# Kernel optimization log

Hardware: AMD Instinct MI355X
Metric: run time of the kernel (lower is better)

## Reference

```python
import jax, jax.numpy as jnp
import numpy as np

B, C, L, H, K, NCONV = 16, 128, 1024, 8, 7, 4
DK = C // H
EPS = 1e-5
NEG = -1e30


def setup_inputs() -> dict:
    key = jax.random.key(0)
    ks = jax.random.split(key, 20)
    s = 0.05
    rn = lambda k, shape: jax.random.normal(k, shape, jnp.float32) * s
    return {
        "x": jax.random.normal(ks[0], (B, C, L), jnp.float32),
        "mask": jax.random.bernoulli(ks[1], 0.1, (B, L)),
        "dw_w": rn(ks[2], (NCONV, C, K)),
        "pw_w": rn(ks[3], (NCONV, C, C)),
        "pw_b": rn(ks[4], (NCONV, C)),
        "ng": jnp.ones((NCONV + 2, C), jnp.float32),
        "nb": jnp.zeros((NCONV + 2, C), jnp.float32),
        "wq": rn(ks[5], (C, C)), "bq": rn(ks[6], (C,)),
        "wk": rn(ks[7], (C, C)), "bk": rn(ks[8], (C,)),
        "wv": rn(ks[9], (C, C)), "bv": rn(ks[10], (C,)),
        "wo": rn(ks[11], (C, C)), "bo": rn(ks[12], (C,)),
        "w1": rn(ks[13], (C, C)), "b1": rn(ks[14], (C,)),
        "w2": rn(ks[15], (C, C)), "b2": rn(ks[16], (C,)),
    }


def _pos_encoding(c, length):
    i = jnp.arange(c, dtype=jnp.float32)
    even = (jnp.arange(c) % 2) == 0
    freq = jnp.where(even, jnp.power(10000.0, -i / c), -jnp.power(10000.0, (1.0 - i) / c))
    phase = jnp.where(even, 0.0, jnp.pi / 2)
    pos = jnp.arange(length, dtype=jnp.float32)
    return jnp.sin(pos[None, :] * freq[:, None] + phase[:, None])  # [C, L]


def _ln(x, g, b):
    # layer norm over channel dim of [B, C, L]
    mu = jnp.mean(x, axis=1, keepdims=True)
    var = jnp.mean(jnp.square(x - mu), axis=1, keepdims=True)
    xn = (x - mu) * jax.lax.rsqrt(var + EPS)
    return xn * g[None, :, None] + b[None, :, None]


def _dsconv(x, dw, pw, pb):
    # depthwise conv1d (groups=C, pad k//2, no bias) + pointwise conv1d (bias)
    y = jax.lax.conv_general_dilated(
        x, dw[:, None, :], window_strides=(1,), padding=[(K // 2, K // 2)],
        feature_group_count=C, dimension_numbers=("NCH", "OIH", "NCH"))
    return jnp.einsum("oc,bcl->bol", pw, y) + pb[None, :, None]


def _attention(x, mask, wq, bq, wk, bk, wv, bv, wo, bo):
    # x: [B, C, L] -> [B, L, C]
    xt = jnp.swapaxes(x, 1, 2)
    q = (xt @ wq.T + bq).reshape(B, L, H, DK)
    k = (xt @ wk.T + bk).reshape(B, L, H, DK)
    v = (xt @ wv.T + bv).reshape(B, L, H, DK)
    scale = 1.0 / np.sqrt(DK)
    scores = jnp.einsum("blhd,bmhd->bhlm", q, k) * scale  # [B, H, L, L]
    scores = jnp.where(mask[:, None, None, :], NEG, scores)
    attn = jax.nn.softmax(scores, axis=-1)
    out = jnp.einsum("bhlm,bmhd->blhd", attn, v).reshape(B, L, C)
    out = out @ wo.T + bo
    return jnp.swapaxes(out, 1, 2)  # [B, C, L]


def reference(x, mask, dw_w, pw_w, pw_b, ng, nb, wq, bq, wk, bk, wv, bv, wo, bo, w1, b1, w2, b2):
    # eval mode: all dropout / stochastic depth are identity
    out = x + _pos_encoding(C, L)[None]
    for i in range(NCONV):
        res = out
        out = _ln(out, ng[i], nb[i])
        out = _dsconv(out, dw_w[i], pw_w[i], pw_b[i])
        out = jax.nn.relu(out)
        out = out + res
    res = out
    out = _ln(out, ng[NCONV], nb[NCONV])
    out = _attention(out, mask, wq, bq, wk, bk, wv, bv, wo, bo)
    out = out + res
    res = out
    out = _ln(out, ng[NCONV + 1], nb[NCONV + 1])
    ot = jnp.swapaxes(out, 1, 2)
    ot = jax.nn.relu(ot @ w1.T + b1)
    ot = ot @ w2.T + b2
    out = jnp.swapaxes(ot, 1, 2) + res
    return out
```

## Files before the change

kernel.cpp:

```cpp
#include <hip/hip_runtime.h>
#include <math.h>


#define ACT_N   2097152
#define OFF_ACT0 0
#define OFF_ACT1 (ACT_N)
#define OFF_QB   (2*ACT_N)
#define OFF_KB   (3*ACT_N)
#define OFF_VT   (4*ACT_N)
#define OFF_ABF  (5*ACT_N)
#define OFF_MF   (6*ACT_N)
#define OFF_WB   (6*ACT_N + 16384)
#define OFF_DW8  (6*ACT_N + 16384 + 81920)

typedef __attribute__((ext_vector_type(8)))  short bf16x8;
typedef __attribute__((ext_vector_type(16))) float f32x16;
typedef __attribute__((ext_vector_type(4)))  float f32x4;

static __device__ __forceinline__ unsigned int f2bf(float f) {
    unsigned int u = __float_as_uint(f);
    return (u + 0x7fffu + ((u >> 16) & 1u)) >> 16;
}
static __device__ __forceinline__ unsigned int pk2(float a, float b) {
    return f2bf(a) | (f2bf(b) << 16);
}

#define GOFF(row, g) (((row) << 8) + ((((g) ^ ((row) & 15))) << 4))

#define QSCALE 0.3606737602222409f

__global__ __launch_bounds__(256) void k_prep(
    const float* __restrict__ pw, const float* __restrict__ wq,
    const float* __restrict__ wk, const float* __restrict__ wv_,
    const float* __restrict__ wo, const float* __restrict__ w1,
    const float* __restrict__ w2, const unsigned char* __restrict__ mask,
    const float* __restrict__ dwsrc,
    unsigned short* __restrict__ wb, float* __restrict__ maskf,
    float* __restrict__ dw8)
{
    int blk = blockIdx.x, t = threadIdx.x;
    if (blk < 10) {
        const float* src;
        if (blk < 4)       src = pw + blk * 16384;
        else if (blk == 4) src = wq;
        else if (blk == 5) src = wk;
        else if (blk == 6) src = wv_;
        else if (blk == 7) src = wo;
        else if (blk == 8) src = w1;
        else               src = w2;
        unsigned short* dst = wb + blk * 16384;
        for (int i = t * 8; i < 16384; i += 2048) {
            float4 a = *(const float4*)(src + i);
            float4 c = *(const float4*)(src + i + 4);
            uint4 v;
            v.x = pk2(a.x, a.y); v.y = pk2(a.z, a.w);
            v.z = pk2(c.x, c.y); v.w = pk2(c.z, c.w);
            *(uint4*)(dst + i) = v;
        }
    } else if (blk == 10) {
        for (int i = t; i < 16384; i += 256)
            maskf[i] = mask[i] ? -3.0e38f : 0.0f;
    } else {
        for (int i = t; i < 4096; i += 256) {
            int n = i >> 3, tap = i & 7;
            dw8[i] = (tap < 7) ? dwsrc[n * 7 + tap] : 0.0f;
        }
    }
}

__global__ __launch_bounds__(256) void k_pe(const float* __restrict__ x,
                                            float* __restrict__ out)
{
    int i4 = blockIdx.x * 256 + threadIdx.x;
    int base = i4 * 4;
    int l = base & 1023;
    int c = (base >> 10) & 127;
    float e = (float)(c & ~1);
    float fb = exp2f(e * (-13.287712379549449f / 128.0f));
    float freq = (c & 1) ? -fb : fb;
    float ph   = (c & 1) ? 1.5707963267948966f : 0.0f;
    float4 xv = ((const float4*)x)[i4];
    float4 o;
    o.x = xv.x + sinf((float)l * freq + ph);
    o.y = xv.y + sinf((float)(l + 1) * freq + ph);
    o.z = xv.z + sinf((float)(l + 2) * freq + ph);
    o.w = xv.w + sinf((float)(l + 3) * freq + ph);
    ((float4*)out)[i4] = o;
}

__global__ __launch_bounds__(512) void k_conv(
    const float* __restrict__ in, float* __restrict__ out,
    const unsigned short* __restrict__ wb,
    const float* __restrict__ dw8,
    const float* __restrict__ pb,
    const float* __restrict__ g, const float* __restrict__ nbv)
{
    __shared__ unsigned short Wl[16384];
    __shared__ unsigned short Xl[8192];
    __shared__ float part[560];
    __shared__ float muL[70], rsL[70];

    const int b  = blockIdx.x >> 4;
    const int l0 = (blockIdx.x & 15) << 6;
    const int t  = threadIdx.x;
    const int lane = t & 63;
    const int w = __builtin_amdgcn_readfirstlane(t >> 6);
    const float* xb = in + b * 131072;

    {
        const uint4* src = (const uint4*)wb;
        #pragma unroll
        for (int i = 0; i < 4; ++i) {
            int gi = t + i * 512;
            uint4 v = src[gi];
            int row = gi >> 4, c16 = gi & 15;
            *(uint4*)((char*)Wl + GOFF(row, c16)) = v;
        }
    }
    if (t < 280) {
        int col = t >> 2, sl = t & 3;
        int gl = l0 - 3 + col;
        float s = 0.f, ss = 0.f;
        if ((unsigned)gl < 1024u) {
            for (int c = sl * 32; c < sl * 32 + 32; ++c) {
                float v = xb[c * 1024 + gl];
                s += v; ss = fmaf(v, v, ss);
            }
        }
        part[col * 8 + sl * 2]     = s;
        part[col * 8 + sl * 2 + 1] = ss;
    }
    __syncthreads();
    if (t < 70) {
        int gl = l0 - 3 + t;
        if ((unsigned)gl < 1024u) {
            float s  = part[t*8] + part[t*8+2] + part[t*8+4] + part[t*8+6];
            float ss = part[t*8+1] + part[t*8+3] + part[t*8+5] + part[t*8+7];
            float mu = s * 0.0078125f;
            float var = ss * 0.0078125f - mu * mu;
            muL[t] = mu; rsL[t] = rsqrtf(var + 1e-5f);
        } else { muL[t] = 0.f; rsL[t] = 0.f; }
    }
    __syncthreads();

    {
        const int l = lane;
        const int gl = l0 + l;
        float m[7], rf[7], vm[7];
        int pofs[7];
        #pragma unroll
        for (int j = 0; j < 7; ++j) {
            int p = gl - 3 + j;
            m[j]  = muL[l + j];
            rf[j] = rsL[l + j];
            vm[j] = ((unsigned)p < 1024u) ? 1.f : 0.f;
            pofs[j] = min(max(p, 0), 1023);
        }
        #pragma unroll
        for (int s = 0; s < 2; ++s) {
            int c0 = w * 16 + s * 8;
            unsigned int pk[4];
            #pragma unroll
            for (int cp = 0; cp < 4; ++cp) {
                float y2[2];
                #pragma unroll
                for (int ci = 0; ci < 2; ++ci) {
                    int c = c0 + cp * 2 + ci;
                    const float* xr = xb + c * 1024;
                    const float* dr = dw8 + c * 8;
                    float S1 = 0.f, S2 = 0.f;
                    #pragma unroll
                    for (int j = 0; j < 7; ++j) {
                        float xv = xr[pofs[j]];
                        float u = (xv - m[j]) * rf[j];
                        float dwv = dr[j];
                        S1 = fmaf(dwv, u,     S1);
                        S2 = fmaf(dwv, vm[j], S2);
                    }
                    y2[ci] = g[c] * S1 + nbv[c] * S2;
                }
                pk[cp] = pk2(y2[0], y2[1]);
            }
            *(uint4*)((char*)Xl + GOFF(l, (c0 >> 3))) = *(uint4*)pk;
        }
    }
    __syncthreads();

    const int l31 = lane & 31, hi = lane >> 5;
    const int ow = w >> 1, lh = w & 1;
    bf16x8 af[8];
    #pragma unroll
    for (int kc = 0; kc < 8; ++kc)
        af[kc] = *(const bf16x8*)((char*)Wl + GOFF(ow * 32 + l31, kc * 2 + hi));
    f32x16 acc;
    #pragma unroll
    for (int i = 0; i < 16; ++i) acc[i] = 0.f;
    #pragma unroll
    for (int kc = 0; kc < 8; ++kc) {
        bf16x8 bx = *(const bf16x8*)((char*)Xl + GOFF(lh * 32 + l31, kc * 2 + hi));
        acc = __builtin_amdgcn_mfma_f32_32x32x16_bf16(af[kc], bx, acc, 0, 0, 0);
    }
    float* ob = out + b * 131072;
    const int lg = l0 + lh * 32 + l31;
    #pragma unroll
    for (int r = 0; r < 16; ++r) {
        int o = ow * 32 + (r & 3) + 8 * (r >> 2) + 4 * hi;
        ob[o * 1024 + lg] = fmaxf(acc[r] + pb[o], 0.f) + xb[o * 1024 + lg];
    }
}

__global__ __launch_bounds__(512) void k_qkv(
    const float* __restrict__ in, const unsigned short* __restrict__ wb,
    const float* __restrict__ bq, const float* __restrict__ bk,
    const float* __restrict__ bv,
    const float* __restrict__ g, const float* __restrict__ nbv,
    unsigned short* __restrict__ qb, unsigned short* __restrict__ kb,
    unsigned short* __restrict__ vt)
{
    __shared__ unsigned short Wl[16384];
    __shared__ unsigned short Xl[8192];
    __shared__ unsigned short vs[8][1280];
    __shared__ float part[1024];
    __shared__ float muL[64], rsL[64];

    const int b  = blockIdx.x >> 4;
    const int l0 = (blockIdx.x & 15) << 6;
    const int t  = threadIdx.x;
    const int lane = t & 63;
    const int w = __builtin_amdgcn_readfirstlane(t >> 6);
    const float* xb = in + b * 131072;

    {
        const uint4* src = (const uint4*)wb;
        #pragma unroll
        for (int i = 0; i < 4; ++i) {
            int gi = t + i * 512;
            uint4 v = src[gi];
            int row = gi >> 4, c16 = gi & 15;
            *(uint4*)((char*)Wl + GOFF(row, c16)) = v;
        }
    }
    {
        int col = t >> 3, sl = t & 7;
        float s = 0.f, ss = 0.f;
        for (int c = sl * 16; c < sl * 16 + 16; ++c) {
            float v = xb[c * 1024 + l0 + col];
            s += v; ss = fmaf(v, v, ss);
        }
        part[col * 16 + sl * 2]     = s;
        part[col * 16 + sl * 2 + 1] = ss;
    }
    __syncthreads();
    if (t < 64) {
        float s = 0.f, ss = 0.f;
        #pragma unroll
        for (int j = 0; j < 8; ++j) { s += part[t*16 + j*2]; ss += part[t*16 + j*2 + 1]; }
        float mu = s * 0.0078125f;
        float var = ss * 0.0078125f - mu * mu;
        muL[t] = mu; rsL[t] = rsqrtf(var + 1e-5f);
    }
    __syncthreads();
    {
        const int l = lane;
        float mu = muL[l], rs = rsL[l];
        #pragma unroll
        for (int s = 0; s < 2; ++s) {
            int c0 = w * 16 + s * 8;
            unsigned int pk[4];
            #pragma unroll
            for (int cp = 0; cp < 4; ++cp) {
                int c = c0 + cp * 2;
                float v0 = (xb[c * 1024 + l0 + l]       - mu) * rs * g[c]     + nbv[c];
                float v1 = (xb[(c + 1) * 1024 + l0 + l] - mu) * rs * g[c + 1] + nbv[c + 1];
                pk[cp] = pk2(v0, v1);
            }
            *(uint4*)((char*)Xl + GOFF(l, (c0 >> 3))) = *(uint4*)pk;
        }
    }
    __syncthreads();

    const int l31 = lane & 31, hi = lane >> 5;
    const int ow = w >> 1, lh = w & 1;
    const int lg = l0 + lh * 32 + l31;

    for (int p = 0; p < 3; ++p) {
        uint4 pw4[4];
        if (p < 2) {
            const uint4* src = (const uint4*)(wb + (p + 1) * 16384);
            #pragma unroll
            for (int i = 0; i < 4; ++i) pw4[i] = src[t + i * 512];
        }
        bf16x8 af[8];
        #pragma unroll
        for (int kc = 0; kc < 8; ++kc)
            af[kc] = *(const bf16x8*)((char*)Wl + GOFF(ow * 32 + l31, kc * 2 + hi));
        f32x16 acc;
        #pragma unroll
        for (int i = 0; i < 16; ++i) acc[i] = 0.f;
        #pragma unroll
        for (int kc = 0; kc < 8; ++kc) {
            bf16x8 bx = *(const bf16x8*)((char*)Xl + GOFF(lh * 32 + l31, kc * 2 + hi));
            acc = __builtin_amdgcn_mfma_f32_32x32x16_bf16(af[kc], bx, acc, 0, 0, 0);
        }

        if (p < 2) {
            const float* bias = (p == 0) ? bq : bk;
            unsigned short* dst = (p == 0) ? qb : kb;
            const float scl = (p == 0) ? QSCALE : 1.0f;
            unsigned int pk0[4], pk1[4];
            #pragma unroll
            for (int j2 = 0; j2 < 4; ++j2) {
                int r = j2 * 2;
                int o0 = ow * 32 + (r & 3) + 8 * (r >> 2) + 4 * hi;
                pk0[j2] = pk2((acc[r] + bias[o0]) * scl,
                              (acc[r + 1] + bias[o0 + 1]) * scl);
                int r8 = r + 8;
                int o1 = ow * 32 + (r8 & 3) + 8 * (r8 >> 2) + 4 * hi;
                pk1[j2] = pk2((acc[r8] + bias[o1]) * scl,
                              (acc[r8 + 1] + bias[o1 + 1]) * scl);
            }
            int bh0 = b * 8 + 2 * ow;
            *(uint4*)(dst + ((size_t)bh0 * 1024 + lg) * 16 + hi * 8) = *(uint4*)pk0;
            *(uint4*)(dst + ((size_t)(bh0 + 1) * 1024 + lg) * 16 + hi * 8) = *(uint4*)pk1;
        } else {
            unsigned short* vsw = vs[w];
            #pragma unroll
            for (int r = 0; r < 16; ++r) {
                int orow = (r & 3) + 8 * (r >> 2) + 4 * hi;
                int o = ow * 32 + orow;
                vsw[orow * 40 + l31] = (unsigned short)f2bf(acc[r] + bv[o]);
            }
            int d32 = l31;
            uint4 v0 = *(uint4*)(vsw + d32 * 40 + hi * 16);
            uint4 v1 = *(uint4*)(vsw + d32 * 40 + hi * 16 + 8);
            int head = 2 * ow + (d32 >> 4), dd = d32 & 15;
            unsigned short* vp = vt + ((size_t)(b * 8 + head) * 16 + dd) * 1024
                                    + l0 + lh * 32 + hi * 16;
            *(uint4*)vp = v0; *(uint4*)(vp + 8) = v1;
        }
        __syncthreads();
        if (p < 2) {
            #pragma unroll
            for (int i = 0; i < 4; ++i) {
                int gi = t + i * 512;
                int row = gi >> 4, c16 = gi & 15;
                *(uint4*)((char*)Wl + GOFF(row, c16)) = pw4[i];
            }
            __syncthreads();
        }
    }
}

__global__ __launch_bounds__(256) void k_attn(
    const unsigned short* __restrict__ qb, const unsigned short* __restrict__ kb,
    const unsigned short* __restrict__ vt, const float* __restrict__ madd,
    unsigned short* __restrict__ abf)
{
    __shared__ unsigned short Kl[2][4096];
    __shared__ unsigned short Vl[2][4224];
    __shared__ float Ml[1024];
    __shared__ unsigned int Pl[4][640];

    const int bh = blockIdx.x >> 3;
    const int b  = bh >> 3;
    const int h  = bh & 7;
    const int qbase = (blockIdx.x & 7) << 7;
    const int t = threadIdx.x;
    const int lane = t & 63;
    const int w = t >> 6;
    const int l31 = lane & 31, hi = lane >> 5;
    const int l15 = lane & 15, h2 = lane >> 4;
    const int qw = qbase + w * 32;

    const uint4* ksrc = (const uint4*)(kb + (size_t)bh * 16384);
    const unsigned short* vsrc = vt + (size_t)bh * 16384;

    const int d0v = t >> 5,          ko0 = t & 31;
    const int d1v = (t + 256) >> 5,  ko1 = (t + 256) & 31;
    const int kp0 = t & 1,        kk0 = t >> 1;
    const int kp1 = t & 1,        kk1 = (t + 256) >> 1;

    ((float4*)Ml)[t] = ((const float4*)(madd + b * 1024))[t];

    bf16x8 qf;
    {
        uint4 qv = *(const uint4*)(qb + ((size_t)bh * 1024 + qw + l31) * 16 + hi * 8);
        union { uint4 u; bf16x8 v; } cvt; cvt.u = qv; qf = cvt.v;
    }
    bf16x8 ones;
    #pragma unroll
    for (int i = 0; i < 8; ++i) ones[i] = (short)0x3F80;

    {
        uint4 kr0 = ksrc[t], kr1 = ksrc[t + 256];
        uint4 vr0 = *(const uint4*)(vsrc + d0v * 1024 + ko0 * 8);
        uint4 vr1 = *(const uint4*)(vsrc + d1v * 1024 + ko1 * 8);
        *(uint4*)(&Kl[0][kp0 * 2048 + kk0 * 8]) = kr0;
        *(uint4*)(&Kl[0][kp1 * 2048 + kk1 * 8]) = kr1;
        *(uint4*)(&Vl[0][d0v * 264 + ko0 * 8]) = vr0;
        *(uint4*)(&Vl[0][d1v * 264 + ko1 * 8]) = vr1;
    }
    __syncthreads();

    f32x16 Z;
    #pragma unroll
    for (int i = 0; i < 16; ++i) Z[i] = 0.f;
    f32x4 O0, O1, Os0, Os1;
    #pragma unroll
    for (int i = 0; i < 4; ++i) { O0[i] = 0.f; O1[i] = 0.f; Os0[i] = 0.f; Os1[i] = 0.f; }

    unsigned int* myP = &Pl[w][0];
    int cur = 0;

    for (int ch = 0; ch < 4; ++ch) {
        uint4 kr0, kr1, vr0, vr1;
        if (ch < 3) {
            int cb = (ch + 1) * 512;
            int vb = (ch + 1) * 256;
            kr0 = ksrc[cb + t];
            kr1 = ksrc[cb + t + 256];
            vr0 = *(const uint4*)(vsrc + d0v * 1024 + vb + ko0 * 8);
            vr1 = *(const uint4*)(vsrc + d1v * 1024 + vb + ko1 * 8);
        }
        const unsigned short* Kb = Kl[cur];
        const unsigned short* Vb = Vl[cur];
        const int kgbase = ch * 256;

        #pragma unroll 2
        for (int kc = 0; kc < 8; ++kc) {
            bf16x8 kf = *(const bf16x8*)(Kb + hi * 2048 + (kc * 32 + l31) * 8);
            f32x16 S = __builtin_amdgcn_mfma_f32_32x32x16_bf16(kf, qf, Z, 0, 0, 0);

            #pragma unroll
            for (int rg = 0; rg < 4; ++rg) {
                float4 mm = *(const float4*)(Ml + kgbase + kc * 32 + rg * 8 + hi * 4);
                float p0 = exp2f(S[rg * 4 + 0] + mm.x);
                float p1 = exp2f(S[rg * 4 + 1] + mm.y);
                float p2 = exp2f(S[rg * 4 + 2] + mm.z);
                float p3 = exp2f(S[rg * 4 + 3] + mm.w);
                uint2 pwd;
                pwd.x = __builtin_amdgcn_perm(__float_as_uint(p1),
                                              __float_as_uint(p0), 0x07060302u);
                pwd.y = __builtin_amdgcn_perm(__float_as_uint(p3),
                                              __float_as_uint(p2), 0x07060302u);
                *(uint2*)((char*)myP + l31 * 80 + rg * 16 + hi * 8) = pwd;
            }

            bf16x8 vf  = *(const bf16x8*)(Vb + l15 * 264 + kc * 32 + h2 * 8);
            bf16x8 pa0 = *(const bf16x8*)((const char*)myP + l15 * 80 + h2 * 16);
            bf16x8 pa1 = *(const bf16x8*)((const char*)myP + (16 + l15) * 80 + h2 * 16);
            O0  = __builtin_amdgcn_mfma_f32_16x16x32_bf16(pa0, vf,   O0,  0, 0, 0);
            O1  = __builtin_amdgcn_mfma_f32_16x16x32_bf16(pa1, vf,   O1,  0, 0, 0);
            Os0 = __builtin_amdgcn_mfma_f32_16x16x32_bf16(pa0, ones, Os0, 0, 0, 0);
            Os1 = __builtin_amdgcn_mfma_f32_16x16x32_bf16(pa1, ones, Os1, 0, 0, 0);
        }

        if (ch < 3) {
            __syncthreads();
            int nxt = cur ^ 1;
            *(uint4*)(&Kl[nxt][kp0 * 2048 + kk0 * 8]) = kr0;
            *(uint4*)(&Kl[nxt][kp1 * 2048 + kk1 * 8]) = kr1;
            *(uint4*)(&Vl[nxt][d0v * 264 + ko0 * 8]) = vr0;
            *(uint4*)(&Vl[nxt][d1v * 264 + ko1 * 8]) = vr1;
            __syncthreads();
            cur = nxt;
        }
    }

    unsigned short* myP16 = (unsigned short*)myP;
    #pragma unroll
    for (int r = 0; r < 4; ++r) {
        float i0 = __builtin_amdgcn_rcpf(Os0[r] + 1e-37f);
        float i1 = __builtin_amdgcn_rcpf(Os1[r] + 1e-37f);
        myP16[(h2 * 4 + r) * 20 + l15]        = (unsigned short)f2bf(O0[r] * i0);
        myP16[(16 + h2 * 4 + r) * 20 + l15]   = (unsigned short)f2bf(O1[r] * i1);
    }
    uint4 ov = *(const uint4*)(myP16 + l31 * 20 + hi * 8);
    *(uint4*)(abf + ((size_t)(b * 1024 + qw + l31)) * 128 + h * 16 + hi * 8) = ov;
}

__global__ __launch_bounds__(512) void k_oproj(
    const unsigned short* __restrict__ abf, const unsigned short* __restrict__ wb,
    const float* __restrict__ bo, const float* __restrict__ res,
    float* __restrict__ out)
{
    __shared__ unsigned short Wl[16384];
    __shared__ unsigned short Xl[8192];
    const int b  = blockIdx.x >> 4;
    const int l0 = (blockIdx.x & 15) << 6;
    const int t  = threadIdx.x;
    const int lane = t & 63;
    const int w = __builtin_amdgcn_readfirstlane(t >> 6);

    {
        const uint4* src = (const uint4*)wb;
        #pragma unroll
        for (int i = 0; i < 4; ++i) {
            int gi = t + i * 512;
            uint4 v = src[gi];
            int row = gi >> 4, c16 = gi & 15;
            *(uint4*)((char*)Wl + GOFF(row, c16)) = v;
        }
        #pragma unroll
        for (int i = 0; i < 2; ++i) {
            int gi = t + i * 512;
            int row = gi >> 4, c16 = gi & 15;
            uint4 v = *(const uint4*)(abf + ((size_t)(b * 1024 + l0 + row)) * 128 + c16 * 8);
            *(uint4*)((char*)Xl + GOFF(row, c16)) = v;
        }
    }
    __syncthreads();

    const int l31 = lane & 31, hi = lane >> 5;
    const int ow = w >> 1, lh = w & 1;
    bf16x8 af[8];
    #pragma unroll
    for (int kc = 0; kc < 8; ++kc)
        af[kc] = *(const bf16x8*)((char*)Wl + GOFF(ow * 32 + l31, kc * 2 + hi));
    f32x16 acc;
    #pragma unroll
    for (int i = 0; i < 16; ++i) acc[i] = 0.f;
    #pragma unroll
    for (int kc = 0; kc < 8; ++kc) {
        bf16x8 bx = *(const bf16x8*)((char*)Xl + GOFF(lh * 32 + l31, kc * 2 + hi));
        acc = __builtin_amdgcn_mfma_f32_32x32x16_bf16(af[kc], bx, acc, 0, 0, 0);
    }
    const float* rb = res + b * 131072;
    float* ob = out + b * 131072;
    const int lg = l0 + lh * 32 + l31;
    #pragma unroll
    for (int r = 0; r < 16; ++r) {
        int o = ow * 32 + (r & 3) + 8 * (r >> 2) + 4 * hi;
        ob[o * 1024 + lg] = acc[r] + bo[o] + rb[o * 1024 + lg];
    }
}

__global__ __launch_bounds__(512) void k_ffn(
    const float* __restrict__ in,
    const unsigned short* __restrict__ w1b, const unsigned short* __restrict__ w2b,
    const float* __restrict__ b1, const float* __restrict__ b2,
    const float* __restrict__ g, const float* __restrict__ nbv,
    float* __restrict__ out)
{
    __shared__ unsigned short Wl[16384];
    __shared__ unsigned short Xl[8192];
    __shared__ unsigned short Xl2[8192];
    __shared__ float part[1024];
    __shared__ float muL[64], rsL[64];

    const int b  = blockIdx.x >> 4;
    const int l0 = (blockIdx.x & 15) << 6;
    const int t  = threadIdx.x;
    const int lane = t & 63;
    const int w = __builtin_amdgcn_readfirstlane(t >> 6);
    const float* xb = in + b * 131072;

    {
        const uint4* src = (const uint4*)w1b;
        #pragma unroll
        for (int i = 0; i < 4; ++i) {
            int gi = t + i * 512;
            uint4 v = src[gi];
            int row = gi >> 4, c16 = gi & 15;
            *(uint4*)((char*)Wl + GOFF(row, c16)) = v;
        }
    }
    {
        int col = t >> 3, sl = t & 7;
        float s = 0.f, ss = 0.f;
        for (int c = sl * 16; c < sl * 16 + 16; ++c) {
            float v = xb[c * 1024 + l0 + col];
            s += v; ss = fmaf(v, v, ss);
        }
        part[col * 16 + sl * 2]     = s;
        part[col * 16 + sl * 2 + 1] = ss;
    }
    __syncthreads();
    if (t < 64) {
        float s = 0.f, ss = 0.f;
        #pragma unroll
        for (int j = 0; j < 8; ++j) { s += part[t*16 + j*2]; ss += part[t*16 + j*2 + 1]; }
        float mu = s * 0.0078125f;
        float var = ss * 0.0078125f - mu * mu;
        muL[t] = mu; rsL[t] = rsqrtf(var + 1e-5f);
    }
    __syncthreads();
    {
        const int l = lane;
        float mu = muL[l], rs = rsL[l];
        #pragma unroll
        for (int s = 0; s < 2; ++s) {
            int c0 = w * 16 + s * 8;
            unsigned int pk[4];
            #pragma unroll
            for (int cp = 0; cp < 4; ++cp) {
                int c = c0 + cp * 2;
                float v0 = (xb[c * 1024 + l0 + l]       - mu) * rs * g[c]     + nbv[c];
                float v1 = (xb[(c + 1) * 1024 + l0 + l] - mu) * rs * g[c + 1] + nbv[c + 1];
                pk[cp] = pk2(v0, v1);
            }
            *(uint4*)((char*)Xl + GOFF(l, (c0 >> 3))) = *(uint4*)pk;
        }
    }
    __syncthreads();

    const int l31 = lane & 31, hi = lane >> 5;
    const int ow = w >> 1, lh = w & 1;
    const int lrow = lh * 32 + l31;

    uint4 pw4[4];
    {
        const uint4* src = (const uint4*)w2b;
        #pragma unroll
        for (int i = 0; i < 4; ++i) pw4[i] = src[t + i * 512];
    }
    {
        bf16x8 af[8];
        #pragma unroll
        for (int kc = 0; kc < 8; ++kc)
            af[kc] = *(const bf16x8*)((char*)Wl + GOFF(ow * 32 + l31, kc * 2 + hi));
        f32x16 acc;
        #pragma unroll
        for (int i = 0; i < 16; ++i) acc[i] = 0.f;
        #pragma unroll
        for (int kc = 0; kc < 8; ++kc) {
            bf16x8 bx = *(const bf16x8*)((char*)Xl + GOFF(lrow, kc * 2 + hi));
            acc = __builtin_amdgcn_mfma_f32_32x32x16_bf16(af[kc], bx, acc, 0, 0, 0);
        }
        #pragma unroll
        for (int r = 0; r < 16; ++r) {
            int o = ow * 32 + (r & 3) + 8 * (r >> 2) + 4 * hi;
            float hval = fmaxf(acc[r] + b1[o], 0.f);
            *(unsigned short*)((char*)Xl2 + (lrow << 8)
                + ((((o >> 3) ^ (lrow & 15))) << 4) + ((o & 7) * 2)) =
                (unsigned short)f2bf(hval);
        }
    }
    __syncthreads();
    {
        #pragma unroll
        for (int i = 0; i < 4; ++i) {
            int gi = t + i * 512;
            int row = gi >> 4, c16 = gi & 15;
            *(uint4*)((char*)Wl + GOFF(row, c16)) = pw4[i];
        }
    }
    __syncthreads();
    {
        bf16x8 af[8];
        #pragma unroll
        for (int kc = 0; kc < 8; ++kc)
            af[kc] = *(const bf16x8*)((char*)Wl + GOFF(ow * 32 + l31, kc * 2 + hi));
        f32x16 acc;
        #pragma unroll
        for (int i = 0; i < 16; ++i) acc[i] = 0.f;
        #pragma unroll
        for (int kc = 0; kc < 8; ++kc) {
            bf16x8 bx = *(const bf16x8*)((char*)Xl2 + GOFF(lrow, kc * 2 + hi));
            acc = __builtin_amdgcn_mfma_f32_32x32x16_bf16(af[kc], bx, acc, 0, 0, 0);
        }
        float* ob = out + b * 131072;
        const int lg = l0 + lrow;
        #pragma unroll
        for (int r = 0; r < 16; ++r) {
            int o = ow * 32 + (r & 3) + 8 * (r >> 2) + 4 * hi;
            ob[o * 1024 + lg] = acc[r] + b2[o] + xb[o * 1024 + lg];
        }
    }
}

extern "C" void kernel_launch(void* const* d_in, const int* in_sizes, int n_in,
                              void* d_out, int out_size, void* d_ws, size_t ws_size,
                              hipStream_t stream)
{
    const float* x    = (const float*)d_in[0];
    const unsigned char* mask = (const unsigned char*)d_in[1];
    const float* dw_w = (const float*)d_in[2];
    const float* pw_w = (const float*)d_in[3];
    const float* pw_b = (const float*)d_in[4];
    const float* ng   = (const float*)d_in[5];
    const float* nb   = (const float*)d_in[6];
    const float* wq   = (const float*)d_in[7];
    const float* bq   = (const float*)d_in[8];
    const float* wk   = (const float*)d_in[9];
    const float* bk   = (const float*)d_in[10];
    const float* wv   = (const float*)d_in[11];
    const float* bv   = (const float*)d_in[12];
    const float* wo   = (const float*)d_in[13];
    const float* bo   = (const float*)d_in[14];
    const float* w1   = (const float*)d_in[15];
    const float* b1   = (const float*)d_in[16];
    const float* w2   = (const float*)d_in[17];
    const float* b2   = (const float*)d_in[18];

    float* ws   = (float*)d_ws;
    float* act0 = ws + OFF_ACT0;
    float* act1 = ws + OFF_ACT1;
    unsigned short* qb  = (unsigned short*)(ws + OFF_QB);
    unsigned short* kbp = (unsigned short*)(ws + OFF_KB);
    unsigned short* vtp = (unsigned short*)(ws + OFF_VT);
    unsigned short* abf = (unsigned short*)(ws + OFF_ABF);
    float* mf   = ws + OFF_MF;
    unsigned short* wb = (unsigned short*)(ws + OFF_WB);
    float* dw8  = ws + OFF_DW8;

    k_prep<<<12, 256, 0, stream>>>(pw_w, wq, wk, wv, wo, w1, w2, mask, dw_w,
                                   wb, mf, dw8);
    k_pe<<<2048, 256, 0, stream>>>(x, act0);

    k_conv<<<256, 512, 0, stream>>>(act0, act1, wb + 0 * 16384, dw8 + 0,
                                    pw_b + 0,   ng + 0,   nb + 0);
    k_conv<<<256, 512, 0, stream>>>(act1, act0, wb + 1 * 16384, dw8 + 1024,
                                    pw_b + 128, ng + 128, nb + 128);
    k_conv<<<256, 512, 0, stream>>>(act0, act1, wb + 2 * 16384, dw8 + 2048,
                                    pw_b + 256, ng + 256, nb + 256);
    k_conv<<<256, 512, 0, stream>>>(act1, act0, wb + 3 * 16384, dw8 + 3072,
                                    pw_b + 384, ng + 384, nb + 384);

    k_qkv<<<256, 512, 0, stream>>>(act0, wb + 4 * 16384, bq, bk, bv,
                                   ng + 4 * 128, nb + 4 * 128, qb, kbp, vtp);
    k_attn<<<1024, 256, 0, stream>>>(qb, kbp, vtp, mf, abf);
    k_oproj<<<256, 512, 0, stream>>>(abf, wb + 7 * 16384, bo, act0, act1);
    k_ffn<<<256, 512, 0, stream>>>(act1, wb + 8 * 16384, wb + 9 * 16384,
                                   b1, b2, ng + 5 * 128, nb + 5 * 128,
                                   (float*)d_out);
}
```

Before: 225.7 us.

## Single-buffer attention K/V LDS, fully unroll inner loop, use native exp2 and setprio

The attention kernel drops its double-buffered K/V shared-memory arrays for single buffers. This is safe because the next chunk is already prefetched into registers and written only between two barriers, and it roughly halves K/V LDS use, which may allow more resident blocks per CU. The inner key loop is now fully unrolled, exp2f is replaced by the hardware exp2 builtin, and s_setprio brackets the PV MFMAs so the scheduler favours matrix work. The risks are higher register pressure from the full unroll and slightly less precise exponentials.

Result: faster. 211.5 us (-6.3%).

```diff
diff --git a/kernel.cpp b/kernel.cpp
--- a/kernel.cpp
+++ b/kernel.cpp
@@ -356,8 +356,8 @@
     const unsigned short* __restrict__ vt, const float* __restrict__ madd,
     unsigned short* __restrict__ abf)
 {
-    __shared__ unsigned short Kl[2][4096];
-    __shared__ unsigned short Vl[2][4224];
+    __shared__ unsigned short Kl[4096];
+    __shared__ unsigned short Vl[4224];
     __shared__ float Ml[1024];
     __shared__ unsigned int Pl[4][640];
 
@@ -395,10 +395,10 @@
         uint4 kr0 = ksrc[t], kr1 = ksrc[t + 256];
         uint4 vr0 = *(const uint4*)(vsrc + d0v * 1024 + ko0 * 8);
         uint4 vr1 = *(const uint4*)(vsrc + d1v * 1024 + ko1 * 8);
-        *(uint4*)(&Kl[0][kp0 * 2048 + kk0 * 8]) = kr0;
-        *(uint4*)(&Kl[0][kp1 * 2048 + kk1 * 8]) = kr1;
-        *(uint4*)(&Vl[0][d0v * 264 + ko0 * 8]) = vr0;
-        *(uint4*)(&Vl[0][d1v * 264 + ko1 * 8]) = vr1;
+        *(uint4*)(&Kl[kp0 * 2048 + kk0 * 8]) = kr0;
+        *(uint4*)(&Kl[kp1 * 2048 + kk1 * 8]) = kr1;
+        *(uint4*)(&Vl[d0v * 264 + ko0 * 8]) = vr0;
+        *(uint4*)(&Vl[d1v * 264 + ko1 * 8]) = vr1;
     }
     __syncthreads();
 
@@ -410,7 +410,6 @@
     for (int i = 0; i < 4; ++i) { O0[i] = 0.f; O1[i] = 0.f; Os0[i] = 0.f; Os1[i] = 0.f; }
 
     unsigned int* myP = &Pl[w][0];
-    int cur = 0;
 
     for (int ch = 0; ch < 4; ++ch) {
         uint4 kr0, kr1, vr0, vr1;
@@ -422,22 +421,20 @@
             vr0 = *(const uint4*)(vsrc + d0v * 1024 + vb + ko0 * 8);
             vr1 = *(const uint4*)(vsrc + d1v * 1024 + vb + ko1 * 8);
         }
-        const unsigned short* Kb = Kl[cur];
-        const unsigned short* Vb = Vl[cur];
         const int kgbase = ch * 256;
 
-        #pragma unroll 2
+        #pragma unroll
         for (int kc = 0; kc < 8; ++kc) {
-            bf16x8 kf = *(const bf16x8*)(Kb + hi * 2048 + (kc * 32 + l31) * 8);
+            bf16x8 kf = *(const bf16x8*)(Kl + hi * 2048 + (kc * 32 + l31) * 8);
             f32x16 S = __builtin_amdgcn_mfma_f32_32x32x16_bf16(kf, qf, Z, 0, 0, 0);
 
             #pragma unroll
             for (int rg = 0; rg < 4; ++rg) {
                 float4 mm = *(const float4*)(Ml + kgbase + kc * 32 + rg * 8 + hi * 4);
-                float p0 = exp2f(S[rg * 4 + 0] + mm.x);
-                float p1 = exp2f(S[rg * 4 + 1] + mm.y);
-                float p2 = exp2f(S[rg * 4 + 2] + mm.z);
-                float p3 = exp2f(S[rg * 4 + 3] + mm.w);
+                float p0 = __builtin_amdgcn_exp2f(S[rg * 4 + 0] + mm.x);
+                float p1 = __builtin_amdgcn_exp2f(S[rg * 4 + 1] + mm.y);
+                float p2 = __builtin_amdgcn_exp2f(S[rg * 4 + 2] + mm.z);
+                float p3 = __builtin_amdgcn_exp2f(S[rg * 4 + 3] + mm.w);
                 uint2 pwd;
                 pwd.x = __builtin_amdgcn_perm(__float_as_uint(p1),
                                               __float_as_uint(p0), 0x07060302u);
@@ -446,24 +443,24 @@
                 *(uint2*)((char*)myP + l31 * 80 + rg * 16 + hi * 8) = pwd;
             }
 
-            bf16x8 vf  = *(const bf16x8*)(Vb + l15 * 264 + kc * 32 + h2 * 8);
+            bf16x8 vf  = *(const bf16x8*)(Vl + l15 * 264 + kc * 32 + h2 * 8);
             bf16x8 pa0 = *(const bf16x8*)((const char*)myP + l15 * 80 + h2 * 16);
             bf16x8 pa1 = *(const bf16x8*)((const char*)myP + (16 + l15) * 80 + h2 * 16);
+            __builtin_amdgcn_s_setprio(1);
             O0  = __builtin_amdgcn_mfma_f32_16x16x32_bf16(pa0, vf,   O0,  0, 0, 0);
             O1  = __builtin_amdgcn_mfma_f32_16x16x32_bf16(pa1, vf,   O1,  0, 0, 0);
             Os0 = __builtin_amdgcn_mfma_f32_16x16x32_bf16(pa0, ones, Os0, 0, 0, 0);
             Os1 = __builtin_amdgcn_mfma_f32_16x16x32_bf16(pa1, ones, Os1, 0, 0, 0);
+            __builtin_amdgcn_s_setprio(0);
         }
 
         if (ch < 3) {
             __syncthreads();
-            int nxt = cur ^ 1;
-            *(uint4*)(&Kl[nxt][kp0 * 2048 + kk0 * 8]) = kr0;
-            *(uint4*)(&Kl[nxt][kp1 * 2048 + kk1 * 8]) = kr1;
-            *(uint4*)(&Vl[nxt][d0v * 264 + ko0 * 8]) = vr0;
-            *(uint4*)(&Vl[nxt][d1v * 264 + ko1 * 8]) = vr1;
+            *(uint4*)(&Kl[kp0 * 2048 + kk0 * 8]) = kr0;
+            *(uint4*)(&Kl[kp1 * 2048 + kk1 * 8]) = kr1;
+            *(uint4*)(&Vl[d0v * 264 + ko0 * 8]) = vr0;
+            *(uint4*)(&Vl[d1v * 264 + ko1 * 8]) = vr1;
             __syncthreads();
-            cur = nxt;
         }
     }
 
```
